# Optimization experiments

Hardware: AMD Instinct MI355X
Metric: run time of the kernel (lower is better)

## Reference

```python
import jax, jax.numpy as jnp
import numpy as np

B, L = 2048, 128          # (src,tgt) pairs x walk positions
K = 4                     # num_layers + 1
ENC = 108                 # enc_dim
D2, D3, D4 = 172, 512, 172
NKEYS = 1_000_000         # unique (batch,node,time,sign) keys in nodetime2emb_maps


def setup_inputs() -> dict:
    key = jax.random.key(0)
    ks = jax.random.split(key, 8)
    emb_table = jax.random.uniform(ks[0], (NKEYS, 2, K), dtype=jnp.float32)
    idx = jax.random.randint(ks[1], (B, L), 0, NKEYS, dtype=jnp.int32)
    W1 = jax.random.normal(ks[2], (K, ENC), dtype=jnp.float32) * (1.0 / np.sqrt(K))
    b1 = jnp.zeros((ENC,), dtype=jnp.float32)
    W2 = jax.random.normal(ks[3], (ENC, ENC), dtype=jnp.float32) * (1.0 / np.sqrt(ENC))
    b2 = jnp.zeros((ENC,), dtype=jnp.float32)
    x2 = jax.random.normal(ks[4], (B, L, D2), dtype=jnp.float32)
    fc1_w = jax.random.normal(ks[5], (ENC + D2, D3), dtype=jnp.float32) * (1.0 / np.sqrt(ENC + D2))
    fc1_b = jnp.zeros((D3,), dtype=jnp.float32)
    fc2_w = jax.random.normal(ks[6], (D3, D4), dtype=jnp.float32) * (1.0 / np.sqrt(D3))
    fc2_b = jnp.zeros((D4,), dtype=jnp.float32)
    return {"emb_table": emb_table, "idx": idx, "W1": W1, "b1": b1, "W2": W2,
            "b2": b2, "x2": x2, "fc1_w": fc1_w, "fc1_b": fc1_b,
            "fc2_w": fc2_w, "fc2_b": fc2_b}


def reference(emb_table, idx, W1, b1, W2, b2, x2, fc1_w, fc1_b, fc2_w, fc2_b):
    # --- PositionEncoder.forward: gather per-(node,time) encodings [B,L,2,K]
    enc = emb_table[idx]
    # --- get_trainable_encodings: Linear(K->ENC), ReLU, Linear(ENC->ENC), sum over src/tgt axis
    h = jax.nn.relu(jnp.einsum('blsk,ke->blse', enc, W1) + b1)
    h = jnp.einsum('blse,ef->blsf', h, W2) + b2
    pe = h.sum(axis=-2)                      # [B, L, ENC]
    # --- MergeLayer (edge_embedding_type='concat'): concat + fc1 + ReLU + fc2
    x = jnp.concatenate([pe, x2], axis=-1)   # [B, L, ENC + D2]
    z = jax.nn.relu(x @ fc1_w + fc1_b) @ fc2_w + fc2_b  # [B, L, D4]
    return z
```

## Files before the change

### kernel.cpp

```cpp
#include <hip/hip_runtime.h>
#include <stdint.h>

typedef __bf16 bf16x8 __attribute__((ext_vector_type(8)));
typedef float  f32x4  __attribute__((ext_vector_type(4)));
typedef unsigned short u16x4 __attribute__((ext_vector_type(4)));

#define XROW_B 576
#define HROW_B 1024
#define LDS_SZ 65536
#define WSTG   40960

#define WS_FC1T   0
#define WS_FC2T   294912
#define WS_BIAS   491520

__device__ __forceinline__ unsigned short f2bf(float f) {
  union { float f; unsigned u; } c; c.f = f;
  unsigned u = c.u;
  u += 0x7FFFu + ((u >> 16) & 1u);
  return (unsigned short)(u >> 16);
}

__global__ void POLAR_prep_fc1(const float* __restrict__ W2,
                               const float* __restrict__ fc1_w,
                               const float* __restrict__ fc1_b,
                               const float* __restrict__ b2,
                               unsigned short* __restrict__ fc1t,
                               float* __restrict__ bias_eff) {
  int n = blockIdx.x;
  int k = threadIdx.x;
  float v = 0.f;
  if (k < 108) {
    for (int f = 0; f < 108; ++f) v += W2[k*108 + f] * fc1_w[f*512 + n];
  } else if (k < 280) {
    v = fc1_w[k*512 + n];
  }
  fc1t[n*288 + k] = f2bf(v);
  if (k == 0) {
    float bb = fc1_b[n];
    for (int f = 0; f < 108; ++f) bb += 2.f * b2[f] * fc1_w[f*512 + n];
    bias_eff[n] = bb;
  }
}

__global__ void POLAR_prep_fc2(const float* __restrict__ fc2_w,
                               unsigned short* __restrict__ fc2t) {
  int n = blockIdx.x;
  int k = threadIdx.x;
  float v = (n < 172) ? fc2_w[k*172 + n] : 0.f;
  fc2t[n*512 + k] = f2bf(v);
}

__global__ __launch_bounds__(512, 4) void POLAR_fused(
    const float* __restrict__ emb, const int* __restrict__ idx,
    const float* __restrict__ W1, const float* __restrict__ b1,
    const float* __restrict__ x2,
    const unsigned short* __restrict__ fc1t,
    const float* __restrict__ bias_eff,
    const unsigned short* __restrict__ fc2t,
    const float* __restrict__ fc2b,
    float* __restrict__ out)
{
  __shared__ __attribute__((aligned(16))) char smem[LDS_SZ];
  const int tid  = threadIdx.x;
  const int lane = tid & 63;
  const int w    = tid >> 6;
  const int blk  = blockIdx.x;
  const int l15  = lane & 15;
  const int l4   = lane >> 4;

  const char* fb1 = (const char*)fc1t;
  const char* fb2 = (const char*)fc2t;

  unsigned boff1[4];
  bf16x8 bva[4], bvb[4];
  #pragma unroll
  for (int j = 0; j < 4; ++j) {
    boff1[j] = (unsigned)((w * 64 + j * 16 + l15) * 576 + l4 * 16);
    bva[j] = *(const bf16x8*)(fb1 + boff1[j]);
  }

  const int r  = tid >> 3;
  const int li = tid & 7;
  int key = idx[(size_t)blk * 64 + r];
  const float* ep = emb + (size_t)key * 8;
  f32x4 e0 = *(const f32x4*)ep;
  f32x4 e1 = *(const f32x4*)(ep + 4);

  {
    float* wsl = (float*)(smem + WSTG);
    if (tid < 432) wsl[tid] = W1[tid];
    else if (tid < 540) wsl[tid] = b1[tid - 432];
    int t2 = tid + 512;
    if (t2 < 540) wsl[t2] = b1[t2 - 432];
  }
  __syncthreads();

  {
    const float* Ws = (const float*)(smem + WSTG);
    unsigned sw = ((unsigned)(r >> 1) & 3u) << 4;
    for (int e = li; e < 108; e += 8) {
      float w0 = Ws[e], w1v = Ws[108 + e], w2v = Ws[216 + e], w3v = Ws[324 + e];
      float bb = Ws[432 + e];
      float a0 = fmaxf(e0.x*w0 + e0.y*w1v + e0.z*w2v + e0.w*w3v + bb, 0.f);
      float a1 = fmaxf(e1.x*w0 + e1.y*w1v + e1.z*w2v + e1.w*w3v + bb, 0.f);
      *(unsigned short*)(smem + r * XROW_B + ((unsigned)(2*e) ^ sw)) = f2bf(a0 + a1);
    }
  }

  {
    const f32x4* x2v = (const f32x4*)(x2 + (size_t)blk * 64 * 172);
    #pragma unroll 1
    for (int t = tid; t < 64 * 43; t += 512) {
      int rr = t / 43, c4 = t - rr * 43;
      f32x4 v = x2v[t];
      u16x4 s; s.x = f2bf(v.x); s.y = f2bf(v.y); s.z = f2bf(v.z); s.w = f2bf(v.w);
      unsigned be = 216u + 8u * (unsigned)c4;
      unsigned sw = ((unsigned)(rr >> 1) & 3u) << 4;
      *(u16x4*)(smem + rr * XROW_B + (be ^ sw)) = s;
    }
    if (tid < 64) {
      unsigned sw = ((unsigned)(tid >> 1) & 3u) << 4;
      union { long2 l; } z; z.l.x = 0; z.l.y = 0;
      *(long2*)(smem + tid * XROW_B + (560u ^ sw)) = z.l;
    }
  }
  __syncthreads();

  f32x4 acc[4][4];
  #pragma unroll
  for (int i = 0; i < 4; ++i)
    #pragma unroll
    for (int j = 0; j < 4; ++j)
      acc[i][j] = (f32x4){0.f, 0.f, 0.f, 0.f};

  unsigned abase[4];
  #pragma unroll
  for (int i = 0; i < 4; ++i) {
    int row = i * 16 + l15;
    abase[i] = (unsigned)(row * XROW_B)
             + (((unsigned)(l4 * 16)) ^ ((((unsigned)row >> 1) & 3u) << 4));
  }

  bf16x8 af[4];
  #pragma unroll 1
  for (int kt = 0; kt < 8; kt += 2) {
    #pragma unroll
    for (int j = 0; j < 4; ++j)
      bvb[j] = *(const bf16x8*)(fb1 + boff1[j] + (kt + 1) * 64);
    #pragma unroll
    for (int i = 0; i < 4; ++i)
      af[i] = *(const bf16x8*)(smem + abase[i] + kt * 64);
    #pragma unroll
    for (int i = 0; i < 4; ++i)
      #pragma unroll
      for (int j = 0; j < 4; ++j)
        acc[i][j] = __builtin_amdgcn_mfma_f32_16x16x32_bf16(af[i], bva[j], acc[i][j], 0, 0, 0);
    #pragma unroll
    for (int j = 0; j < 4; ++j)
      bva[j] = *(const bf16x8*)(fb1 + boff1[j] + (kt + 2) * 64);
    #pragma unroll
    for (int i = 0; i < 4; ++i)
      af[i] = *(const bf16x8*)(smem + abase[i] + (kt + 1) * 64);
    #pragma unroll
    for (int i = 0; i < 4; ++i)
      #pragma unroll
      for (int j = 0; j < 4; ++j)
        acc[i][j] = __builtin_amdgcn_mfma_f32_16x16x32_bf16(af[i], bvb[j], acc[i][j], 0, 0, 0);
  }
  {
    #pragma unroll
    for (int i = 0; i < 4; ++i)
      af[i] = *(const bf16x8*)(smem + abase[i] + 8 * 64);
    #pragma unroll
    for (int i = 0; i < 4; ++i)
      #pragma unroll
      for (int j = 0; j < 4; ++j)
        acc[i][j] = __builtin_amdgcn_mfma_f32_16x16x32_bf16(af[i], bva[j], acc[i][j], 0, 0, 0);
  }
  __syncthreads();

  const int wm4 = w >> 2;
  const int wn4 = w & 3;
  unsigned boff2[3];
  bf16x8 b2a[3][2], b2b[3][2];
  #pragma unroll
  for (int j = 0; j < 3; ++j) {
    boff2[j] = (unsigned)((wn4 * 48 + j * 16 + l15) * 1024 + l4 * 16);
    #pragma unroll
    for (int s = 0; s < 2; ++s)
      b2a[j][s] = *(const bf16x8*)(fb2 + boff2[j] + s * 64);
  }

  {
    const int odd = lane & 1;
    #pragma unroll
    for (int i = 0; i < 4; ++i) {
      #pragma unroll
      for (int j = 0; j < 4; ++j) {
        int col0 = w * 64 + j * 16 + l15;
        float be = bias_eff[col0];
        float a0 = fmaxf(acc[i][j][0] + be, 0.f);
        float a1 = fmaxf(acc[i][j][1] + be, 0.f);
        float a2 = fmaxf(acc[i][j][2] + be, 0.f);
        float a3 = fmaxf(acc[i][j][3] + be, 0.f);
        float t0 = odd ? a0 : a2;
        float t1 = odd ? a1 : a3;
        float p0 = __shfl_xor(t0, 1);
        float p1 = __shfl_xor(t1, 1);
        unsigned w0 = odd ? ((unsigned)f2bf(p0) | ((unsigned)f2bf(a2) << 16))
                          : ((unsigned)f2bf(a0) | ((unsigned)f2bf(p0) << 16));
        unsigned w1 = odd ? ((unsigned)f2bf(p1) | ((unsigned)f2bf(a3) << 16))
                          : ((unsigned)f2bf(a1) | ((unsigned)f2bf(p1) << 16));
        int row0 = i * 16 + l4 * 4 + (odd ? 2 : 0);
        int row1 = row0 + 1;
        unsigned cb = (unsigned)((col0 & ~1) * 2);
        *(unsigned*)(smem + row0 * HROW_B + (cb ^ (((unsigned)row0 & 7u) << 4))) = w0;
        *(unsigned*)(smem + row1 * HROW_B + (cb ^ (((unsigned)row1 & 7u) << 4))) = w1;
      }
    }
  }
  __syncthreads();

  f32x4 acc2[2][3];
  #pragma unroll
  for (int i = 0; i < 2; ++i)
    #pragma unroll
    for (int j = 0; j < 3; ++j)
      acc2[i][j] = (f32x4){0.f, 0.f, 0.f, 0.f};

  unsigned h0base[2], swr2[2];
  #pragma unroll
  for (int i = 0; i < 2; ++i) {
    int row = wm4 * 32 + i * 16 + l15;
    h0base[i] = (unsigned)(row * HROW_B);
    swr2[i] = (((unsigned)row & 7u) << 4);
  }

  bf16x8 a2[2][2];
  #pragma unroll 1
  for (int kt = 0; kt < 8; kt += 2) {
    #pragma unroll
    for (int j = 0; j < 3; ++j)
      #pragma unroll
      for (int s = 0; s < 2; ++s)
        b2b[j][s] = *(const bf16x8*)(fb2 + boff2[j] + (kt + 1) * 128 + s * 64);
    #pragma unroll
    for (int i = 0; i < 2; ++i)
      #pragma unroll
      for (int s = 0; s < 2; ++s)
        a2[i][s] = *(const bf16x8*)(smem + h0base[i]
                     + (((unsigned)(kt * 128 + s * 64 + l4 * 16)) ^ swr2[i]));
    #pragma unroll
    for (int s = 0; s < 2; ++s)
      #pragma unroll
      for (int i = 0; i < 2; ++i)
        #pragma unroll
        for (int j = 0; j < 3; ++j)
          acc2[i][j] = __builtin_amdgcn_mfma_f32_16x16x32_bf16(a2[i][s], b2a[j][s], acc2[i][j], 0, 0, 0);
    if (kt < 6) {
      #pragma unroll
      for (int j = 0; j < 3; ++j)
        #pragma unroll
        for (int s = 0; s < 2; ++s)
          b2a[j][s] = *(const bf16x8*)(fb2 + boff2[j] + (kt + 2) * 128 + s * 64);
    }
    #pragma unroll
    for (int i = 0; i < 2; ++i)
      #pragma unroll
      for (int s = 0; s < 2; ++s)
        a2[i][s] = *(const bf16x8*)(smem + h0base[i]
                     + (((unsigned)((kt + 1) * 128 + s * 64 + l4 * 16)) ^ swr2[i]));
    #pragma unroll
    for (int s = 0; s < 2; ++s)
      #pragma unroll
      for (int i = 0; i < 2; ++i)
        #pragma unroll
        for (int j = 0; j < 3; ++j)
          acc2[i][j] = __builtin_amdgcn_mfma_f32_16x16x32_bf16(a2[i][s], b2b[j][s], acc2[i][j], 0, 0, 0);
  }

  const size_t orow0 = (size_t)blk * 64;
  #pragma unroll
  for (int j = 0; j < 3; ++j) {
    int col = wn4 * 48 + j * 16 + l15;
    if (col < 172) {
      float bias = fc2b[col];
      #pragma unroll
      for (int i = 0; i < 2; ++i) {
        #pragma unroll
        for (int r2 = 0; r2 < 4; ++r2) {
          int row = wm4 * 32 + i * 16 + l4 * 4 + r2;
          out[(orow0 + row) * 172 + col] = acc2[i][j][r2] + bias;
        }
      }
    }
  }
}

extern "C" void kernel_launch(void* const* d_in, const int* in_sizes, int n_in,
                              void* d_out, int out_size, void* d_ws, size_t ws_size,
                              hipStream_t stream) {
  (void)in_sizes; (void)n_in; (void)out_size; (void)ws_size;
  const float* emb   = (const float*)d_in[0];
  const int*   idx   = (const int*)d_in[1];
  const float* W1    = (const float*)d_in[2];
  const float* b1    = (const float*)d_in[3];
  const float* W2    = (const float*)d_in[4];
  const float* b2    = (const float*)d_in[5];
  const float* x2    = (const float*)d_in[6];
  const float* fc1_w = (const float*)d_in[7];
  const float* fc1_b = (const float*)d_in[8];
  const float* fc2_w = (const float*)d_in[9];
  const float* fc2_b = (const float*)d_in[10];
  float* out = (float*)d_out;
  char* ws = (char*)d_ws;
  unsigned short* fc1t = (unsigned short*)(ws + WS_FC1T);
  unsigned short* fc2t = (unsigned short*)(ws + WS_FC2T);
  float* bias_eff = (float*)(ws + WS_BIAS);

  POLAR_prep_fc1<<<512, 288, 0, stream>>>(W2, fc1_w, fc1_b, b2, fc1t, bias_eff);
  POLAR_prep_fc2<<<192, 512, 0, stream>>>(fc2_w, fc2t);
  POLAR_fused<<<4096, 512, 0, stream>>>(emb, idx, W1, b1, x2, fc1t, bias_eff,
                                        fc2t, fc2_b, out);
}
```

Before: 350.2 us.

## Split fused kernel into row-prep and GEMM kernels with bf16 staging buffer

Moves the embedding gather, first-layer encoding and x2 bf16 conversion into a separate kernel that writes pre-swizzled bf16 tiles to a workspace buffer. The GEMM kernel then bulk-loads those tiles into LDS, raises wave priority around MFMA blocks, and uses nontemporal output stores. The goal is to pull latency-bound gather and convert work out of the MFMA kernel. The cost is an extra launch and a round trip of about 150MB of bf16 staging data through memory.

```diff
diff --git a/kernel.cpp b/kernel.cpp
--- a/kernel.cpp
+++ b/kernel.cpp
@@ -8,11 +8,14 @@
 #define XROW_B 576
 #define HROW_B 1024
 #define LDS_SZ 65536
-#define WSTG   40960
+
+#define RLDS_W  36864
+#define RLDS_SZ 39040
 
 #define WS_FC1T   0
 #define WS_FC2T   294912
 #define WS_BIAS   491520
+#define WS_XBF    524288
 
 __device__ __forceinline__ unsigned short f2bf(float f) {
   union { float f; unsigned u; } c; c.f = f;
@@ -51,10 +54,76 @@
   fc2t[n*512 + k] = f2bf(v);
 }
 
-__global__ __launch_bounds__(512, 4) void POLAR_fused(
+__global__ __launch_bounds__(512) void POLAR_rows(
     const float* __restrict__ emb, const int* __restrict__ idx,
     const float* __restrict__ W1, const float* __restrict__ b1,
-    const float* __restrict__ x2,
+    const float* __restrict__ x2, unsigned short* __restrict__ xbf)
+{
+  __shared__ __attribute__((aligned(16))) char rsm[RLDS_SZ];
+  const int tid = threadIdx.x, blk = blockIdx.x;
+
+  const int p = tid >> 3, q = tid & 7;
+  const size_t row = (size_t)blk * 64 + p;
+  int key = idx[row];
+  const float* ep = emb + (size_t)key * 8;
+  f32x4 e0 = *(const f32x4*)ep;
+  f32x4 e1 = *(const f32x4*)(ep + 4);
+
+  float* wsl = (float*)(rsm + RLDS_W);
+  for (int tt = tid; tt < 540; tt += 512)
+    wsl[tt] = (tt < 432) ? W1[tt] : b1[tt - 432];
+  __syncthreads();
+
+  {
+    unsigned sw = ((unsigned)(p >> 1) & 3u) << 4;
+    char* xr = rsm + p * XROW_B;
+    #pragma unroll
+    for (int i2 = 0; i2 < 7; ++i2) {
+      int e = q * 14 + 2 * i2;
+      if (e < 108) {
+        float wa0 = wsl[e],   wa1 = wsl[108+e], wa2 = wsl[216+e], wa3 = wsl[324+e], ba = wsl[432+e];
+        float wb0 = wsl[e+1], wb1 = wsl[109+e], wb2 = wsl[217+e], wb3 = wsl[325+e], bb = wsl[433+e];
+        float a = fmaxf(e0.x*wa0 + e0.y*wa1 + e0.z*wa2 + e0.w*wa3 + ba, 0.f)
+                + fmaxf(e1.x*wa0 + e1.y*wa1 + e1.z*wa2 + e1.w*wa3 + ba, 0.f);
+        float b = fmaxf(e0.x*wb0 + e0.y*wb1 + e0.z*wb2 + e0.w*wb3 + bb, 0.f)
+                + fmaxf(e1.x*wb0 + e1.y*wb1 + e1.z*wb2 + e1.w*wb3 + bb, 0.f);
+        unsigned pk = (unsigned)f2bf(a) | ((unsigned)f2bf(b) << 16);
+        *(unsigned*)(xr + ((unsigned)(2 * e) ^ sw)) = pk;
+      }
+    }
+  }
+
+  {
+    const f32x4* x2v = (const f32x4*)(x2 + (size_t)blk * 64 * 172);
+    #pragma unroll 1
+    for (int tt = tid; tt < 64 * 43; tt += 512) {
+      int rr = tt / 43, c4 = tt - rr * 43;
+      f32x4 v = x2v[tt];
+      u16x4 s; s.x = f2bf(v.x); s.y = f2bf(v.y); s.z = f2bf(v.z); s.w = f2bf(v.w);
+      unsigned sw = ((unsigned)(rr >> 1) & 3u) << 4;
+      *(u16x4*)(rsm + rr * XROW_B + ((216u + 8u * (unsigned)c4) ^ sw)) = s;
+    }
+    if (tid < 64) {
+      unsigned sw = ((unsigned)(tid >> 1) & 3u) << 4;
+      f32x4 z = (f32x4){0.f, 0.f, 0.f, 0.f};
+      *(f32x4*)(rsm + tid * XROW_B + (560u ^ sw)) = z;
+    }
+  }
+  __syncthreads();
+
+  {
+    f32x4* dst = (f32x4*)((char*)xbf + (size_t)blk * 36864);
+    const f32x4* src = (const f32x4*)rsm;
+    #pragma unroll
+    for (int k2 = 0; k2 < 4; ++k2)
+      __builtin_nontemporal_store(src[tid + k2 * 512], &dst[tid + k2 * 512]);
+    if (tid < 256)
+      __builtin_nontemporal_store(src[tid + 2048], &dst[tid + 2048]);
+  }
+}
+
+__global__ __launch_bounds__(512, 4) void POLAR_gemm(
+    const unsigned short* __restrict__ xbf,
     const unsigned short* __restrict__ fc1t,
     const float* __restrict__ bias_eff,
     const unsigned short* __restrict__ fc2t,
@@ -72,6 +141,14 @@
   const char* fb1 = (const char*)fc1t;
   const char* fb2 = (const char*)fc2t;
 
+  const f32x4* xsrc = (const f32x4*)((const char*)xbf + (size_t)blk * 36864);
+  f32x4 xv0 = __builtin_nontemporal_load(xsrc + tid);
+  f32x4 xv1 = __builtin_nontemporal_load(xsrc + tid + 512);
+  f32x4 xv2 = __builtin_nontemporal_load(xsrc + tid + 1024);
+  f32x4 xv3 = __builtin_nontemporal_load(xsrc + tid + 1536);
+  f32x4 xv4 = (tid < 256) ? __builtin_nontemporal_load(xsrc + tid + 2048)
+                          : (f32x4){0.f, 0.f, 0.f, 0.f};
+
   unsigned boff1[4];
   bf16x8 bva[4], bvb[4];
   #pragma unroll
@@ -80,50 +157,13 @@
     bva[j] = *(const bf16x8*)(fb1 + boff1[j]);
   }
 
-  const int r  = tid >> 3;
-  const int li = tid & 7;
-  int key = idx[(size_t)blk * 64 + r];
-  const float* ep = emb + (size_t)key * 8;
-  f32x4 e0 = *(const f32x4*)ep;
-  f32x4 e1 = *(const f32x4*)(ep + 4);
-
-  {
-    float* wsl = (float*)(smem + WSTG);
-    if (tid < 432) wsl[tid] = W1[tid];
-    else if (tid < 540) wsl[tid] = b1[tid - 432];
-    int t2 = tid + 512;
-    if (t2 < 540) wsl[t2] = b1[t2 - 432];
-  }
-  __syncthreads();
-
-  {
-    const float* Ws = (const float*)(smem + WSTG);
-    unsigned sw = ((unsigned)(r >> 1) & 3u) << 4;
-    for (int e = li; e < 108; e += 8) {
-      float w0 = Ws[e], w1v = Ws[108 + e], w2v = Ws[216 + e], w3v = Ws[324 + e];
-      float bb = Ws[432 + e];
-      float a0 = fmaxf(e0.x*w0 + e0.y*w1v + e0.z*w2v + e0.w*w3v + bb, 0.f);
-      float a1 = fmaxf(e1.x*w0 + e1.y*w1v + e1.z*w2v + e1.w*w3v + bb, 0.f);
-      *(unsigned short*)(smem + r * XROW_B + ((unsigned)(2*e) ^ sw)) = f2bf(a0 + a1);
-    }
-  }
-
-  {
-    const f32x4* x2v = (const f32x4*)(x2 + (size_t)blk * 64 * 172);
-    #pragma unroll 1
-    for (int t = tid; t < 64 * 43; t += 512) {
-      int rr = t / 43, c4 = t - rr * 43;
-      f32x4 v = x2v[t];
-      u16x4 s; s.x = f2bf(v.x); s.y = f2bf(v.y); s.z = f2bf(v.z); s.w = f2bf(v.w);
-      unsigned be = 216u + 8u * (unsigned)c4;
-      unsigned sw = ((unsigned)(rr >> 1) & 3u) << 4;
-      *(u16x4*)(smem + rr * XROW_B + (be ^ sw)) = s;
-    }
-    if (tid < 64) {
-      unsigned sw = ((unsigned)(tid >> 1) & 3u) << 4;
-      union { long2 l; } z; z.l.x = 0; z.l.y = 0;
-      *(long2*)(smem + tid * XROW_B + (560u ^ sw)) = z.l;
-    }
+  {
+    f32x4* sx = (f32x4*)smem;
+    sx[tid] = xv0;
+    sx[tid + 512] = xv1;
+    sx[tid + 1024] = xv2;
+    sx[tid + 1536] = xv3;
+    if (tid < 256) sx[tid + 2048] = xv4;
   }
   __syncthreads();
 
@@ -151,32 +191,38 @@
     #pragma unroll
     for (int i = 0; i < 4; ++i)
       af[i] = *(const bf16x8*)(smem + abase[i] + kt * 64);
+    __builtin_amdgcn_s_setprio(1);
     #pragma unroll
     for (int i = 0; i < 4; ++i)
       #pragma unroll
       for (int j = 0; j < 4; ++j)
         acc[i][j] = __builtin_amdgcn_mfma_f32_16x16x32_bf16(af[i], bva[j], acc[i][j], 0, 0, 0);
+    __builtin_amdgcn_s_setprio(0);
     #pragma unroll
     for (int j = 0; j < 4; ++j)
       bva[j] = *(const bf16x8*)(fb1 + boff1[j] + (kt + 2) * 64);
     #pragma unroll
     for (int i = 0; i < 4; ++i)
       af[i] = *(const bf16x8*)(smem + abase[i] + (kt + 1) * 64);
+    __builtin_amdgcn_s_setprio(1);
     #pragma unroll
     for (int i = 0; i < 4; ++i)
       #pragma unroll
       for (int j = 0; j < 4; ++j)
         acc[i][j] = __builtin_amdgcn_mfma_f32_16x16x32_bf16(af[i], bvb[j], acc[i][j], 0, 0, 0);
+    __builtin_amdgcn_s_setprio(0);
   }
   {
     #pragma unroll
     for (int i = 0; i < 4; ++i)
       af[i] = *(const bf16x8*)(smem + abase[i] + 8 * 64);
+    __builtin_amdgcn_s_setprio(1);
     #pragma unroll
     for (int i = 0; i < 4; ++i)
       #pragma unroll
       for (int j = 0; j < 4; ++j)
         acc[i][j] = __builtin_amdgcn_mfma_f32_16x16x32_bf16(af[i], bva[j], acc[i][j], 0, 0, 0);
+    __builtin_amdgcn_s_setprio(0);
   }
   __syncthreads();
 
@@ -251,6 +297,7 @@
       for (int s = 0; s < 2; ++s)
         a2[i][s] = *(const bf16x8*)(smem + h0base[i]
                      + (((unsigned)(kt * 128 + s * 64 + l4 * 16)) ^ swr2[i]));
+    __builtin_amdgcn_s_setprio(1);
     #pragma unroll
     for (int s = 0; s < 2; ++s)
       #pragma unroll
@@ -258,6 +305,7 @@
         #pragma unroll
         for (int j = 0; j < 3; ++j)
           acc2[i][j] = __builtin_amdgcn_mfma_f32_16x16x32_bf16(a2[i][s], b2a[j][s], acc2[i][j], 0, 0, 0);
+    __builtin_amdgcn_s_setprio(0);
     if (kt < 6) {
       #pragma unroll
       for (int j = 0; j < 3; ++j)
@@ -271,6 +319,7 @@
       for (int s = 0; s < 2; ++s)
         a2[i][s] = *(const bf16x8*)(smem + h0base[i]
                      + (((unsigned)((kt + 1) * 128 + s * 64 + l4 * 16)) ^ swr2[i]));
+    __builtin_amdgcn_s_setprio(1);
     #pragma unroll
     for (int s = 0; s < 2; ++s)
       #pragma unroll
@@ -278,6 +327,7 @@
         #pragma unroll
         for (int j = 0; j < 3; ++j)
           acc2[i][j] = __builtin_amdgcn_mfma_f32_16x16x32_bf16(a2[i][s], b2b[j][s], acc2[i][j], 0, 0, 0);
+    __builtin_amdgcn_s_setprio(0);
   }
 
   const size_t orow0 = (size_t)blk * 64;
@@ -291,7 +341,8 @@
         #pragma unroll
         for (int r2 = 0; r2 < 4; ++r2) {
           int row = wm4 * 32 + i * 16 + l4 * 4 + r2;
-          out[(orow0 + row) * 172 + col] = acc2[i][j][r2] + bias;
+          __builtin_nontemporal_store(acc2[i][j][r2] + bias,
+                                      &out[(orow0 + row) * 172 + col]);
         }
       }
     }
@@ -318,9 +369,10 @@
   unsigned short* fc1t = (unsigned short*)(ws + WS_FC1T);
   unsigned short* fc2t = (unsigned short*)(ws + WS_FC2T);
   float* bias_eff = (float*)(ws + WS_BIAS);
+  unsigned short* xbf  = (unsigned short*)(ws + WS_XBF);
 
   POLAR_prep_fc1<<<512, 288, 0, stream>>>(W2, fc1_w, fc1_b, b2, fc1t, bias_eff);
   POLAR_prep_fc2<<<192, 512, 0, stream>>>(fc2_w, fc2t);
-  POLAR_fused<<<4096, 512, 0, stream>>>(emb, idx, W1, b1, x2, fc1t, bias_eff,
-                                        fc2t, fc2_b, out);
-}
+  POLAR_rows<<<4096, 512, 0, stream>>>(emb, idx, W1, b1, x2, xbf);
+  POLAR_gemm<<<4096, 512, 0, stream>>>(xbf, fc1t, bias_eff, fc2t, fc2_b, out);
+}
```

After: 473.1 us. 1.35x slower.
